# Performance work log

Measured on AMD Instinct MI355X. Metric: run time of the kernel, lower is better.

The kernel has to match this reference:

```python
import jax, jax.numpy as jnp
import numpy as np

CHANNEL = 1
ALPHA = 1.0
EPS = 1e-10
SHAPE = (1, CHANNEL, 160, 192, 160)


def _sobel_kernels(channel):
    s2 = np.array([[-1., 0., 1.], [-2., 0., 2.], [-1., 0., 1.]], dtype=np.float32)
    # sobel.repeat(channel,1,3,1,1): 2D kernel tiled along depth -> k[d,h,w] = s2[h,w]
    kx = np.tile(s2[None, :, :], (3, 1, 1))
    ky = np.tile(s2.T[None, :, :], (3, 1, 1))
    kz = np.array([[[-1., -1., -1.], [-2., -2., -2.], [-1., -1., -1.]],
                   [[0., 0., 0.], [0., 0., 0.], [0., 0., 0.]],
                   [[1., 1., 1.], [2., 2., 2.], [1., 1., 1.]]], dtype=np.float32)
    def rep(k):  # -> [channel, 1, 3, 3, 3] for depthwise conv
        return jnp.asarray(np.tile(k[None, None], (channel, 1, 1, 1, 1)))
    return rep(kx), rep(ky), rep(kz)


def _conv3d(x, k, channel):
    # torch F.conv3d (cross-correlation), padding=1, groups=channel
    return jax.lax.conv_general_dilated(
        x, k, window_strides=(1, 1, 1), padding=((1, 1), (1, 1), (1, 1)),
        dimension_numbers=('NCDHW', 'OIDHW', 'NCDHW'),
        feature_group_count=channel)


def setup_inputs() -> dict:
    key = jax.random.key(0)
    k1, k2, k3 = jax.random.split(key, 3)
    M = jax.random.normal(k1, SHAPE, dtype=jnp.float32)
    S = jax.random.normal(k2, SHAPE, dtype=jnp.float32)
    flow = jax.random.normal(k3, (SHAPE[0], 3) + SHAPE[2:], dtype=jnp.float32)
    return {"M": M, "S": S, "flow": flow}


def reference(M, S, flow):
    kx, ky, kz = _sobel_kernels(CHANNEL)
    Idiff = M - S
    Sx = _conv3d(S, kx, CHANNEL)
    Sy = _conv3d(S, ky, CHANNEL)
    Sz = _conv3d(S, kz, CHANNEL)
    Mx = _conv3d(M, kx, CHANNEL)
    My = _conv3d(M, ky, CHANNEL)
    Mz = _conv3d(M, kz, CHANNEL)
    Sxyz_mag = Sx ** 2 + Sy ** 2 + Sz ** 2
    Mxyz_mag = Mx ** 2 + My ** 2 + Mz ** 2
    denom_S = Sxyz_mag + (ALPHA ** 2) * Idiff ** 2 + 1e-10
    denom_M = Mxyz_mag + (ALPHA ** 2) * Idiff ** 2 + 1e-10
    Ux = Idiff * (Sx / denom_S + Mx / denom_M)
    Uy = Idiff * (Sy / denom_S + My / denom_M)
    Uz = Idiff * (Sz / denom_S + Mz / denom_M)
    demons_ori_xz = jnp.arctan(Ux / (Uz + EPS))
    demons_ori_yz = jnp.arctan(Uy / (Uz + EPS))
    flow_ori_xz = jnp.arctan(flow[:, 0] / (flow[:, 2] + EPS))
    flow_ori_yz = jnp.arctan(flow[:, 1] / (flow[:, 2] + EPS))
    ori_error = jnp.mean((flow_ori_xz - demons_ori_xz) ** 2) + \
                jnp.mean((flow_ori_yz - demons_ori_yz) ** 2)
    return ori_error
```

## Files before the change

kernel.cpp:

```cpp
#include <hip/hip_runtime.h>
#include <math.h>

#define DD 160
#define HH 192
#define WW 160
#define TW 32
#define TH 8
#define TD 8
#define HW (HH * WW)
#define NVOX (DD * HW)
#define HTW 34
#define HTH 10
#define HALO (HTW * HTH)

__device__ __forceinline__ float atan_fast(float r) {
    float ar = fabsf(r);
    float inv = __builtin_amdgcn_rcpf(ar);
    bool big = ar > 1.0f;
    float x = big ? inv : ar;
    float x2 = x * x;
    float p = fmaf(x2, fmaf(x2, fmaf(x2, fmaf(x2, fmaf(x2,
              -0.0117212f, 0.05265332f), -0.11643287f), 0.19354346f),
              -0.33262347f), 0.99997726f);
    p *= x;
    float res = big ? (1.57079632679489662f - p) : p;
    return copysignf(res, r);
}

__global__ __launch_bounds__(256) void demons_ori_kernel(
    const float* __restrict__ Mv, const float* __restrict__ Sv,
    const float* __restrict__ flow, float* __restrict__ out)
{
    __shared__ float buf[2][2][HTH][HTW];
    __shared__ float redbuf[4];

    const int tid = threadIdx.x;
    const int tw = tid & 31;
    const int th = tid >> 5;
    const int w0 = blockIdx.x * TW;
    const int h0 = blockIdx.y * TH;
    const int d0 = blockIdx.z * TD;

    const bool has1 = (tid < HALO - 256);
    int idx0, gb0, idx1 = 0, gb1 = 0;
    bool ok0, ok1 = false;
    {
        int i = tid;
        int hh = i / HTW, ww = i - HTW * hh;
        int gh = h0 + hh - 1, gw = w0 + ww - 1;
        idx0 = i;
        ok0 = (gh >= 0 && gh < HH && gw >= 0 && gw < WW);
        gb0 = gh * WW + gw;
        if (has1) {
            i = tid + 256;
            hh = i / HTW; ww = i - HTW * hh;
            gh = h0 + hh - 1; gw = w0 + ww - 1;
            idx1 = i;
            ok1 = (gh >= 0 && gh < HH && gw >= 0 && gw < WW);
            gb1 = gh * WW + gw;
        }
    }

    float pS0 = 0.f, pM0 = 0.f, pS1 = 0.f, pM1 = 0.f;

    auto issue = [&](int d) {
        const bool din = (d >= 0) && (d < DD);
        const size_t base = (size_t)d * HW;
        pS0 = (din && ok0) ? Sv[base + gb0] : 0.f;
        pM0 = (din && ok0) ? Mv[base + gb0] : 0.f;
        pS1 = (din && ok1) ? Sv[base + gb1] : 0.f;
        pM1 = (din && ok1) ? Mv[base + gb1] : 0.f;
    };
    auto commit = [&](int d) {
        float* __restrict__ bS = &buf[d & 1][0][0][0];
        float* __restrict__ bM = &buf[d & 1][1][0][0];
        bS[idx0] = pS0;
        bM[idx0] = pM0;
        if (has1) { bS[idx1] = pS1; bM[idx1] = pM1; }
    };

    const int hc = th + 1, wc = tw + 1;
    auto partials = [&](int par, float pq[2][4]) {
        #pragma unroll
        for (int f = 0; f < 2; ++f) {
            const float* __restrict__ b = &buf[par][f][0][0];
            const float* r0 = b + (hc - 1) * HTW + (wc - 1);
            const float* r1 = r0 + HTW;
            const float* r2 = r1 + HTW;
            float v00 = r0[0], v01 = r0[1], v02 = r0[2];
            float v10 = r1[0], v11 = r1[1], v12 = r1[2];
            float v20 = r2[0], v21 = r2[1], v22 = r2[2];
            pq[f][0] = (v02 + 2.f * v12 + v22) - (v00 + 2.f * v10 + v20);
            pq[f][1] = (v20 + 2.f * v21 + v22) - (v00 + 2.f * v01 + v02);
            pq[f][2] = (v00 + v01 + v02) + 2.f * (v10 + v11 + v12)
                     + (v20 + v21 + v22);
            pq[f][3] = v11;
        }
    };

    float Pm[2][4], P0[2][4], Pp[2][4];

    issue(d0 - 1);
    commit(d0 - 1);
    issue(d0);
    __syncthreads();
    partials((d0 - 1) & 1, Pm);
    commit(d0);
    issue(d0 + 1);
    __syncthreads();
    partials(d0 & 1, P0);

    const size_t voff0 = (size_t)(h0 + th) * WW + (w0 + tw);
    float fFx = flow[(size_t)d0 * HW + voff0];
    float fFy = flow[(size_t)NVOX + (size_t)d0 * HW + voff0];
    float fFz = flow[2 * (size_t)NVOX + (size_t)d0 * HW + voff0];

    float lsum = 0.f;

    #pragma unroll
    for (int dd = 0; dd < TD; ++dd) {
        const int d = d0 + dd;
        commit(d + 1);
        float nFx = 0.f, nFy = 0.f, nFz = 0.f;
        if (dd < TD - 1) {
            issue(d + 2);
            size_t foff = (size_t)(d + 1) * HW + voff0;
            nFx = flow[foff];
            nFy = flow[(size_t)NVOX + foff];
            nFz = flow[2 * (size_t)NVOX + foff];
        }
        __syncthreads();
        partials((d + 1) & 1, Pp);

        float idf = P0[1][3] - P0[0][3];
        float i2 = idf * idf + 1e-10f;
        float gxS = Pm[0][0] + P0[0][0] + Pp[0][0];
        float gyS = Pm[0][1] + P0[0][1] + Pp[0][1];
        float gzS = Pp[0][2] - Pm[0][2];
        float gxM = Pm[1][0] + P0[1][0] + Pp[1][0];
        float gyM = Pm[1][1] + P0[1][1] + Pp[1][1];
        float gzM = Pp[1][2] - Pm[1][2];
        float denS = gxS * gxS + gyS * gyS + gzS * gzS + i2;
        float denM = gxM * gxM + gyM * gyM + gzM * gzM + i2;
        float rS = __builtin_amdgcn_rcpf(denS);
        float rM = __builtin_amdgcn_rcpf(denM);
        float Ux = idf * (gxS * rS + gxM * rM);
        float Uy = idf * (gyS * rS + gyM * rM);
        float Uz = idf * (gzS * rS + gzM * rM);
        float rz = __builtin_amdgcn_rcpf(Uz + 1e-10f);
        float dxz = atan_fast(Ux * rz);
        float dyz = atan_fast(Uy * rz);

        float rf = __builtin_amdgcn_rcpf(fFz + 1e-10f);
        float fxz = atan_fast(fFx * rf);
        float fyz = atan_fast(fFy * rf);

        float e1 = fxz - dxz;
        float e2 = fyz - dyz;
        lsum += e1 * e1 + e2 * e2;

        #pragma unroll
        for (int f = 0; f < 2; ++f)
            #pragma unroll
            for (int q = 0; q < 4; ++q) {
                Pm[f][q] = P0[f][q];
                P0[f][q] = Pp[f][q];
            }
        fFx = nFx; fFy = nFy; fFz = nFz;
    }

    #pragma unroll
    for (int o = 32; o > 0; o >>= 1)
        lsum += __shfl_down(lsum, o, 64);
    if ((tid & 63) == 0)
        redbuf[tid >> 6] = lsum;
    __syncthreads();
    if (tid == 0) {
        float s = redbuf[0] + redbuf[1] + redbuf[2] + redbuf[3];
        atomicAdd(out, s * (1.0f / (float)NVOX));
    }
}

extern "C" void kernel_launch(void* const* d_in, const int* in_sizes, int n_in,
                              void* d_out, int out_size, void* d_ws, size_t ws_size,
                              hipStream_t stream) {
    const float* Mv   = (const float*)d_in[0];
    const float* Sv   = (const float*)d_in[1];
    const float* flow = (const float*)d_in[2];
    float* out = (float*)d_out;

    hipMemsetAsync(out, 0, sizeof(float), stream);

    dim3 grid(WW / TW, HH / TH, DD / TD);
    demons_ori_kernel<<<grid, dim3(256), 0, stream>>>(Mv, Sv, flow, out);
}
```

Baseline: 140.9 us.

## Use single-wave blocks with smaller tiles and slotted atomic reduction

Shrinks each block to one 64-thread wavefront over a 16x4 tile marching 16 depth slices, with padded LDS row stride. It drops the cross-wave shared-memory reduction and spreads the per-block atomics over 64 padded workspace slots, which a second tiny kernel sums. The aim is less atomic contention on a single address and more, lighter blocks for occupancy. In exchange the smaller tile has a larger halo-to-interior ratio, so more redundant global loads, and it adds a second kernel launch.

```diff
diff --git a/kernel.cpp b/kernel.cpp
--- a/kernel.cpp
+++ b/kernel.cpp
@@ -4,14 +4,16 @@
 #define DD 160
 #define HH 192
 #define WW 160
-#define TW 32
-#define TH 8
-#define TD 8
+#define TW 16
+#define TH 4
+#define TD 16
 #define HW (HH * WW)
 #define NVOX (DD * HW)
-#define HTW 34
-#define HTH 10
-#define HALO (HTW * HTH)
+#define HTW 18
+#define HTH 6
+#define LSTR 20
+#define HALO (HTH * HTW)
+#define NSLOT 64
 
 __device__ __forceinline__ float atan_fast(float r) {
     float ar = fabsf(r);
@@ -27,35 +29,34 @@
     return copysignf(res, r);
 }
 
-__global__ __launch_bounds__(256) void demons_ori_kernel(
+__global__ __launch_bounds__(64) void demons_ori_kernel(
     const float* __restrict__ Mv, const float* __restrict__ Sv,
-    const float* __restrict__ flow, float* __restrict__ out)
+    const float* __restrict__ flow, float* __restrict__ ws)
 {
-    __shared__ float buf[2][2][HTH][HTW];
-    __shared__ float redbuf[4];
+    __shared__ float buf[2][2][HTH * LSTR];
 
     const int tid = threadIdx.x;
-    const int tw = tid & 31;
-    const int th = tid >> 5;
+    const int tw = tid & 15;
+    const int th = tid >> 4;
     const int w0 = blockIdx.x * TW;
     const int h0 = blockIdx.y * TH;
     const int d0 = blockIdx.z * TD;
 
-    const bool has1 = (tid < HALO - 256);
+    const bool has1 = (tid < HALO - 64);
     int idx0, gb0, idx1 = 0, gb1 = 0;
     bool ok0, ok1 = false;
     {
         int i = tid;
         int hh = i / HTW, ww = i - HTW * hh;
         int gh = h0 + hh - 1, gw = w0 + ww - 1;
-        idx0 = i;
+        idx0 = hh * LSTR + ww;
         ok0 = (gh >= 0 && gh < HH && gw >= 0 && gw < WW);
         gb0 = gh * WW + gw;
         if (has1) {
-            i = tid + 256;
+            i = tid + 64;
             hh = i / HTW; ww = i - HTW * hh;
             gh = h0 + hh - 1; gw = w0 + ww - 1;
-            idx1 = i;
+            idx1 = hh * LSTR + ww;
             ok1 = (gh >= 0 && gh < HH && gw >= 0 && gw < WW);
             gb1 = gh * WW + gw;
         }
@@ -72,21 +73,21 @@
         pM1 = (din && ok1) ? Mv[base + gb1] : 0.f;
     };
     auto commit = [&](int d) {
-        float* __restrict__ bS = &buf[d & 1][0][0][0];
-        float* __restrict__ bM = &buf[d & 1][1][0][0];
+        float* __restrict__ bS = &buf[d & 1][0][0];
+        float* __restrict__ bM = &buf[d & 1][1][0];
         bS[idx0] = pS0;
         bM[idx0] = pM0;
         if (has1) { bS[idx1] = pS1; bM[idx1] = pM1; }
     };
 
-    const int hc = th + 1, wc = tw + 1;
+    const int rb = th * LSTR + tw;
     auto partials = [&](int par, float pq[2][4]) {
         #pragma unroll
         for (int f = 0; f < 2; ++f) {
-            const float* __restrict__ b = &buf[par][f][0][0];
-            const float* r0 = b + (hc - 1) * HTW + (wc - 1);
-            const float* r1 = r0 + HTW;
-            const float* r2 = r1 + HTW;
+            const float* __restrict__ b = &buf[par][f][0];
+            const float* r0 = b + rb;
+            const float* r1 = r0 + LSTR;
+            const float* r2 = r1 + LSTR;
             float v00 = r0[0], v01 = r0[1], v02 = r0[2];
             float v10 = r1[0], v11 = r1[1], v12 = r1[2];
             float v20 = r2[0], v21 = r2[1], v22 = r2[2];
@@ -117,7 +118,7 @@
 
     float lsum = 0.f;
 
-    #pragma unroll
+    #pragma unroll 4
     for (int dd = 0; dd < TD; ++dd) {
         const int d = d0 + dd;
         commit(d + 1);
@@ -172,13 +173,21 @@
     #pragma unroll
     for (int o = 32; o > 0; o >>= 1)
         lsum += __shfl_down(lsum, o, 64);
-    if ((tid & 63) == 0)
-        redbuf[tid >> 6] = lsum;
-    __syncthreads();
     if (tid == 0) {
-        float s = redbuf[0] + redbuf[1] + redbuf[2] + redbuf[3];
-        atomicAdd(out, s * (1.0f / (float)NVOX));
+        int bid = (blockIdx.z * gridDim.y + blockIdx.y) * gridDim.x + blockIdx.x;
+        atomicAdd(ws + (bid & (NSLOT - 1)) * 32, lsum);
     }
+}
+
+__global__ __launch_bounds__(64) void reduce_kernel(
+    const float* __restrict__ ws, float* __restrict__ out)
+{
+    float v = ws[threadIdx.x * 32];
+    #pragma unroll
+    for (int o = 32; o > 0; o >>= 1)
+        v += __shfl_down(v, o, 64);
+    if (threadIdx.x == 0)
+        out[0] = v * (1.0f / (float)NVOX);
 }
 
 extern "C" void kernel_launch(void* const* d_in, const int* in_sizes, int n_in,
@@ -188,9 +197,11 @@
     const float* Sv   = (const float*)d_in[1];
     const float* flow = (const float*)d_in[2];
     float* out = (float*)d_out;
-
-    hipMemsetAsync(out, 0, sizeof(float), stream);
+    float* ws  = (float*)d_ws;
+
+    hipMemsetAsync(ws, 0, NSLOT * 32 * sizeof(float), stream);
 
     dim3 grid(WW / TW, HH / TH, DD / TD);
-    demons_ori_kernel<<<grid, dim3(256), 0, stream>>>(Mv, Sv, flow, out);
-}
+    demons_ori_kernel<<<grid, dim3(64), 0, stream>>>(Mv, Sv, flow, ws);
+    reduce_kernel<<<dim3(1), dim3(64), 0, stream>>>(ws, out);
+}
```

Result: slower. 144.3 us (+2.4%).

## Give each wavefront a private halo tile and drop block barriers

Applied to the files above, without the earlier changes.

Splits the 32x8 block tile into four 16x4 per-wavefront tiles, each with its own double-buffered shared-memory halo region. Because each wave fills only its own region, the per-slice __syncthreads calls are removed. Loads are also double-buffered in registers two slices ahead, for both the S/M halo and the flow values. The cost is a larger halo overhead per voxel (18x6 halo for 16x4 outputs, versus 34x10 for 32x8), so more redundant global loads, plus extra registers for the second prefetch set. Correctness relies on wave-synchronous execution of LDS writes and reads within a single wavefront, with no explicit barrier.

```diff
diff --git a/kernel.cpp b/kernel.cpp
--- a/kernel.cpp
+++ b/kernel.cpp
@@ -4,14 +4,18 @@
 #define DD 160
 #define HH 192
 #define WW 160
-#define TW 32
-#define TH 8
+#define TW 16
+#define TH 4
+#define BW 32
+#define BH 8
 #define TD 8
 #define HW (HH * WW)
 #define NVOX (DD * HW)
-#define HTW 34
-#define HTH 10
-#define HALO (HTW * HTH)
+#define HTW 18
+#define HTH 6
+#define LSTR 17
+#define HALO (HTH * HTW)
+#define WBUF (HTH * LSTR)
 
 __device__ __forceinline__ float atan_fast(float r) {
     float ar = fabsf(r);
@@ -31,62 +35,78 @@
     const float* __restrict__ Mv, const float* __restrict__ Sv,
     const float* __restrict__ flow, float* __restrict__ out)
 {
-    __shared__ float buf[2][2][HTH][HTW];
+    __shared__ float buf[4][2][2][WBUF];
     __shared__ float redbuf[4];
 
     const int tid = threadIdx.x;
-    const int tw = tid & 31;
-    const int th = tid >> 5;
-    const int w0 = blockIdx.x * TW;
-    const int h0 = blockIdx.y * TH;
+    const int wid = tid >> 6;
+    const int lane = tid & 63;
+    const int tw = lane & 15;
+    const int th = lane >> 4;
+    const int w0 = blockIdx.x * BW + (wid & 1) * TW;
+    const int h0 = blockIdx.y * BH + (wid >> 1) * TH;
     const int d0 = blockIdx.z * TD;
 
-    const bool has1 = (tid < HALO - 256);
+    const bool has1 = (lane < HALO - 64);
     int idx0, gb0, idx1 = 0, gb1 = 0;
     bool ok0, ok1 = false;
     {
-        int i = tid;
+        int i = lane;
         int hh = i / HTW, ww = i - HTW * hh;
         int gh = h0 + hh - 1, gw = w0 + ww - 1;
-        idx0 = i;
+        idx0 = hh * LSTR + ww;
         ok0 = (gh >= 0 && gh < HH && gw >= 0 && gw < WW);
         gb0 = gh * WW + gw;
         if (has1) {
-            i = tid + 256;
+            i = lane + 64;
             hh = i / HTW; ww = i - HTW * hh;
             gh = h0 + hh - 1; gw = w0 + ww - 1;
-            idx1 = i;
+            idx1 = hh * LSTR + ww;
             ok1 = (gh >= 0 && gh < HH && gw >= 0 && gw < WW);
             gb1 = gh * WW + gw;
         }
     }
 
-    float pS0 = 0.f, pM0 = 0.f, pS1 = 0.f, pM1 = 0.f;
-
-    auto issue = [&](int d) {
+    float aS0 = 0.f, aM0 = 0.f, aS1 = 0.f, aM1 = 0.f;
+    float bS0 = 0.f, bM0 = 0.f, bS1 = 0.f, bM1 = 0.f;
+
+    auto issueA = [&](int d) {
         const bool din = (d >= 0) && (d < DD);
         const size_t base = (size_t)d * HW;
-        pS0 = (din && ok0) ? Sv[base + gb0] : 0.f;
-        pM0 = (din && ok0) ? Mv[base + gb0] : 0.f;
-        pS1 = (din && ok1) ? Sv[base + gb1] : 0.f;
-        pM1 = (din && ok1) ? Mv[base + gb1] : 0.f;
-    };
-    auto commit = [&](int d) {
-        float* __restrict__ bS = &buf[d & 1][0][0][0];
-        float* __restrict__ bM = &buf[d & 1][1][0][0];
-        bS[idx0] = pS0;
-        bM[idx0] = pM0;
-        if (has1) { bS[idx1] = pS1; bM[idx1] = pM1; }
-    };
-
-    const int hc = th + 1, wc = tw + 1;
+        aS0 = (din && ok0) ? Sv[base + gb0] : 0.f;
+        aM0 = (din && ok0) ? Mv[base + gb0] : 0.f;
+        aS1 = (din && ok1) ? Sv[base + gb1] : 0.f;
+        aM1 = (din && ok1) ? Mv[base + gb1] : 0.f;
+    };
+    auto issueB = [&](int d) {
+        const bool din = (d >= 0) && (d < DD);
+        const size_t base = (size_t)d * HW;
+        bS0 = (din && ok0) ? Sv[base + gb0] : 0.f;
+        bM0 = (din && ok0) ? Mv[base + gb0] : 0.f;
+        bS1 = (din && ok1) ? Sv[base + gb1] : 0.f;
+        bM1 = (din && ok1) ? Mv[base + gb1] : 0.f;
+    };
+    auto commitA = [&](int d) {
+        float* __restrict__ bS = &buf[wid][d & 1][0][0];
+        float* __restrict__ bM = &buf[wid][d & 1][1][0];
+        bS[idx0] = aS0; bM[idx0] = aM0;
+        if (has1) { bS[idx1] = aS1; bM[idx1] = aM1; }
+    };
+    auto commitB = [&](int d) {
+        float* __restrict__ bS = &buf[wid][d & 1][0][0];
+        float* __restrict__ bM = &buf[wid][d & 1][1][0];
+        bS[idx0] = bS0; bM[idx0] = bM0;
+        if (has1) { bS[idx1] = bS1; bM[idx1] = bM1; }
+    };
+
+    const int rb = th * LSTR + tw;
     auto partials = [&](int par, float pq[2][4]) {
         #pragma unroll
         for (int f = 0; f < 2; ++f) {
-            const float* __restrict__ b = &buf[par][f][0][0];
-            const float* r0 = b + (hc - 1) * HTW + (wc - 1);
-            const float* r1 = r0 + HTW;
-            const float* r2 = r1 + HTW;
+            const float* __restrict__ b = &buf[wid][par][f][0];
+            const float* r0 = b + rb;
+            const float* r1 = r0 + LSTR;
+            const float* r2 = r1 + LSTR;
             float v00 = r0[0], v01 = r0[1], v02 = r0[2];
             float v10 = r1[0], v11 = r1[1], v12 = r1[2];
             float v20 = r2[0], v21 = r2[1], v22 = r2[2];
@@ -100,36 +120,35 @@
 
     float Pm[2][4], P0[2][4], Pp[2][4];
 
-    issue(d0 - 1);
-    commit(d0 - 1);
-    issue(d0);
-    __syncthreads();
+    issueA(d0 - 1);
+    issueB(d0);
+    commitA(d0 - 1);
     partials((d0 - 1) & 1, Pm);
-    commit(d0);
-    issue(d0 + 1);
-    __syncthreads();
+    issueA(d0 + 1);
+    commitB(d0);
     partials(d0 & 1, P0);
+    issueB(d0 + 2);
 
     const size_t voff0 = (size_t)(h0 + th) * WW + (w0 + tw);
-    float fFx = flow[(size_t)d0 * HW + voff0];
-    float fFy = flow[(size_t)NVOX + (size_t)d0 * HW + voff0];
-    float fFz = flow[2 * (size_t)NVOX + (size_t)d0 * HW + voff0];
+    float fx0 = flow[(size_t)d0 * HW + voff0];
+    float fy0 = flow[(size_t)NVOX + (size_t)d0 * HW + voff0];
+    float fz0 = flow[2 * (size_t)NVOX + (size_t)d0 * HW + voff0];
+    float fx1 = flow[(size_t)(d0 + 1) * HW + voff0];
+    float fy1 = flow[(size_t)NVOX + (size_t)(d0 + 1) * HW + voff0];
+    float fz1 = flow[2 * (size_t)NVOX + (size_t)(d0 + 1) * HW + voff0];
 
     float lsum = 0.f;
 
     #pragma unroll
     for (int dd = 0; dd < TD; ++dd) {
         const int d = d0 + dd;
-        commit(d + 1);
-        float nFx = 0.f, nFy = 0.f, nFz = 0.f;
-        if (dd < TD - 1) {
-            issue(d + 2);
-            size_t foff = (size_t)(d + 1) * HW + voff0;
-            nFx = flow[foff];
-            nFy = flow[(size_t)NVOX + foff];
-            nFz = flow[2 * (size_t)NVOX + foff];
-        }
-        __syncthreads();
+        if ((dd & 1) == 0) {
+            commitA(d + 1);
+            if (dd <= TD - 3) issueA(d + 3);
+        } else {
+            commitB(d + 1);
+            if (dd <= TD - 3) issueB(d + 3);
+        }
         partials((d + 1) & 1, Pp);
 
         float idf = P0[1][3] - P0[0][3];
@@ -151,13 +170,29 @@
         float dxz = atan_fast(Ux * rz);
         float dyz = atan_fast(Uy * rz);
 
-        float rf = __builtin_amdgcn_rcpf(fFz + 1e-10f);
-        float fxz = atan_fast(fFx * rf);
-        float fyz = atan_fast(fFy * rf);
+        float ffx = (dd & 1) ? fx1 : fx0;
+        float ffy = (dd & 1) ? fy1 : fy0;
+        float ffz = (dd & 1) ? fz1 : fz0;
+        float rf = __builtin_amdgcn_rcpf(ffz + 1e-10f);
+        float fxz = atan_fast(ffx * rf);
+        float fyz = atan_fast(ffy * rf);
 
         float e1 = fxz - dxz;
         float e2 = fyz - dyz;
         lsum += e1 * e1 + e2 * e2;
+
+        if (dd <= TD - 3) {
+            size_t foff = (size_t)(d + 2) * HW + voff0;
+            if ((dd & 1) == 0) {
+                fx0 = flow[foff];
+                fy0 = flow[(size_t)NVOX + foff];
+                fz0 = flow[2 * (size_t)NVOX + foff];
+            } else {
+                fx1 = flow[foff];
+                fy1 = flow[(size_t)NVOX + foff];
+                fz1 = flow[2 * (size_t)NVOX + foff];
+            }
+        }
 
         #pragma unroll
         for (int f = 0; f < 2; ++f)
@@ -166,14 +201,13 @@
                 Pm[f][q] = P0[f][q];
                 P0[f][q] = Pp[f][q];
             }
-        fFx = nFx; fFy = nFy; fFz = nFz;
     }
 
     #pragma unroll
     for (int o = 32; o > 0; o >>= 1)
         lsum += __shfl_down(lsum, o, 64);
-    if ((tid & 63) == 0)
-        redbuf[tid >> 6] = lsum;
+    if (lane == 0)
+        redbuf[wid] = lsum;
     __syncthreads();
     if (tid == 0) {
         float s = redbuf[0] + redbuf[1] + redbuf[2] + redbuf[3];
@@ -191,6 +225,6 @@
 
     hipMemsetAsync(out, 0, sizeof(float), stream);
 
-    dim3 grid(WW / TW, HH / TH, DD / TD);
+    dim3 grid(WW / BW, HH / BH, DD / TD);
     demons_ori_kernel<<<grid, dim3(256), 0, stream>>>(Mv, Sv, flow, out);
 }
```

Result: slower. 145.1 us (+3.0%).

## Give each wavefront a private halo tile to drop block-wide barriers

Applied to the files above, without the earlier changes.

Splits the 32x8 block tile into four 16x4 per-wavefront sub-tiles, each with its own double-buffered 18x6 shared-memory halo (padded stride 24). Each wavefront loads and consumes only its own halo, so the per-depth-slice __syncthreads calls are removed. Halo overhead grows (18x6 per 64 voxels versus 34x10 per 256), which means more redundant global and LDS traffic. Correctness relies on lockstep execution within a wavefront and compiler ordering of the LDS writes and reads without an explicit barrier.

```diff
diff --git a/kernel.cpp b/kernel.cpp
--- a/kernel.cpp
+++ b/kernel.cpp
@@ -4,14 +4,18 @@
 #define DD 160
 #define HH 192
 #define WW 160
-#define TW 32
-#define TH 8
+#define TW 16
+#define TH 4
+#define BW 32
+#define BH 8
 #define TD 8
 #define HW (HH * WW)
 #define NVOX (DD * HW)
-#define HTW 34
-#define HTH 10
-#define HALO (HTW * HTH)
+#define HTW 18
+#define HTH 6
+#define LSTR 24
+#define HALO (HTH * HTW)
+#define WBUF (HTH * LSTR)
 
 __device__ __forceinline__ float atan_fast(float r) {
     float ar = fabsf(r);
@@ -31,31 +35,33 @@
     const float* __restrict__ Mv, const float* __restrict__ Sv,
     const float* __restrict__ flow, float* __restrict__ out)
 {
-    __shared__ float buf[2][2][HTH][HTW];
+    __shared__ float buf[4][2][2][WBUF];
     __shared__ float redbuf[4];
 
     const int tid = threadIdx.x;
-    const int tw = tid & 31;
-    const int th = tid >> 5;
-    const int w0 = blockIdx.x * TW;
-    const int h0 = blockIdx.y * TH;
+    const int wid = tid >> 6;
+    const int lane = tid & 63;
+    const int tw = lane & 15;
+    const int th = lane >> 4;
+    const int w0 = blockIdx.x * BW + (wid & 1) * TW;
+    const int h0 = blockIdx.y * BH + (wid >> 1) * TH;
     const int d0 = blockIdx.z * TD;
 
-    const bool has1 = (tid < HALO - 256);
+    const bool has1 = (lane < HALO - 64);
     int idx0, gb0, idx1 = 0, gb1 = 0;
     bool ok0, ok1 = false;
     {
-        int i = tid;
+        int i = lane;
         int hh = i / HTW, ww = i - HTW * hh;
         int gh = h0 + hh - 1, gw = w0 + ww - 1;
-        idx0 = i;
+        idx0 = hh * LSTR + ww;
         ok0 = (gh >= 0 && gh < HH && gw >= 0 && gw < WW);
         gb0 = gh * WW + gw;
         if (has1) {
-            i = tid + 256;
+            i = lane + 64;
             hh = i / HTW; ww = i - HTW * hh;
             gh = h0 + hh - 1; gw = w0 + ww - 1;
-            idx1 = i;
+            idx1 = hh * LSTR + ww;
             ok1 = (gh >= 0 && gh < HH && gw >= 0 && gw < WW);
             gb1 = gh * WW + gw;
         }
@@ -72,21 +78,20 @@
         pM1 = (din && ok1) ? Mv[base + gb1] : 0.f;
     };
     auto commit = [&](int d) {
-        float* __restrict__ bS = &buf[d & 1][0][0][0];
-        float* __restrict__ bM = &buf[d & 1][1][0][0];
-        bS[idx0] = pS0;
-        bM[idx0] = pM0;
+        float* __restrict__ bS = &buf[wid][d & 1][0][0];
+        float* __restrict__ bM = &buf[wid][d & 1][1][0];
+        bS[idx0] = pS0; bM[idx0] = pM0;
         if (has1) { bS[idx1] = pS1; bM[idx1] = pM1; }
     };
 
-    const int hc = th + 1, wc = tw + 1;
+    const int rb = th * LSTR + tw;
     auto partials = [&](int par, float pq[2][4]) {
         #pragma unroll
         for (int f = 0; f < 2; ++f) {
-            const float* __restrict__ b = &buf[par][f][0][0];
-            const float* r0 = b + (hc - 1) * HTW + (wc - 1);
-            const float* r1 = r0 + HTW;
-            const float* r2 = r1 + HTW;
+            const float* __restrict__ b = &buf[wid][par][f][0];
+            const float* r0 = b + rb;
+            const float* r1 = r0 + LSTR;
+            const float* r2 = r1 + LSTR;
             float v00 = r0[0], v01 = r0[1], v02 = r0[2];
             float v10 = r1[0], v11 = r1[1], v12 = r1[2];
             float v20 = r2[0], v21 = r2[1], v22 = r2[2];
@@ -103,11 +108,9 @@
     issue(d0 - 1);
     commit(d0 - 1);
     issue(d0);
-    __syncthreads();
     partials((d0 - 1) & 1, Pm);
     commit(d0);
     issue(d0 + 1);
-    __syncthreads();
     partials(d0 & 1, P0);
 
     const size_t voff0 = (size_t)(h0 + th) * WW + (w0 + tw);
@@ -129,7 +132,6 @@
             nFy = flow[(size_t)NVOX + foff];
             nFz = flow[2 * (size_t)NVOX + foff];
         }
-        __syncthreads();
         partials((d + 1) & 1, Pp);
 
         float idf = P0[1][3] - P0[0][3];
@@ -172,8 +174,8 @@
     #pragma unroll
     for (int o = 32; o > 0; o >>= 1)
         lsum += __shfl_down(lsum, o, 64);
-    if ((tid & 63) == 0)
-        redbuf[tid >> 6] = lsum;
+    if (lane == 0)
+        redbuf[wid] = lsum;
     __syncthreads();
     if (tid == 0) {
         float s = redbuf[0] + redbuf[1] + redbuf[2] + redbuf[3];
@@ -191,6 +193,6 @@
 
     hipMemsetAsync(out, 0, sizeof(float), stream);
 
-    dim3 grid(WW / TW, HH / TH, DD / TD);
+    dim3 grid(WW / BW, HH / BH, DD / TD);
     demons_ori_kernel<<<grid, dim3(256), 0, stream>>>(Mv, Sv, flow, out);
 }
```

Measured after the change: 152.3 us. +8.1%, slower.
